# Performance work log

Measured on AMD Instinct MI355X. Metric: run time of the kernel, lower is better.

Reference implementation:

```python
import jax, jax.numpy as jnp
import numpy as np

B, LF, RATE = 2, 2048, 4
DF, DS, H = 1024, 1024, 8
D2 = DF // 2            # 512: both self (d1) and cross (d2) branch dims (equal split)
POOL_H = 2048
TS = LF // RATE         # 512 slow steps


def _p(key, shape):
    return jax.random.normal(key, shape, jnp.float32) * 0.02


def setup_inputs() -> dict:
    keys = iter(jax.random.split(jax.random.key(0), 32))
    inp = {
        "x_fast": jax.random.normal(next(keys), (B, LF, DF), jnp.float32),
        "x_slow": jax.random.normal(next(keys), (B, TS, DS), jnp.float32),
    }
    for name in ("fself", "fcross", "sself", "scross"):
        inp[f"{name}_wqkv"] = _p(next(keys), (D2, 3 * D2))
        inp[f"{name}_bqkv"] = jnp.zeros((3 * D2,), jnp.float32)
        inp[f"{name}_wo"] = _p(next(keys), (D2, D2))
        inp[f"{name}_bo"] = jnp.zeros((D2,), jnp.float32)
    inp["lift_w"] = _p(next(keys), (DS, D2))
    inp["lift_b"] = jnp.zeros((D2,), jnp.float32)
    inp["pool_w1"] = _p(next(keys), (RATE * DF, POOL_H))
    inp["pool_b1"] = jnp.zeros((POOL_H,), jnp.float32)
    inp["pool_w2"] = _p(next(keys), (POOL_H, D2))
    inp["pool_b2"] = jnp.zeros((D2,), jnp.float32)
    return inp


def _mha(q_in, k_in, v_in, wqkv, bqkv, wo, bo):
    """Standard multihead attention with fused in-proj weight [d, 3d]."""
    b, tq, d = q_in.shape
    hd = d // H
    q = q_in @ wqkv[:, :d] + bqkv[:d]
    k = k_in @ wqkv[:, d:2 * d] + bqkv[d:2 * d]
    v = v_in @ wqkv[:, 2 * d:] + bqkv[2 * d:]
    q = q.reshape(b, tq, H, hd)
    k = k.reshape(b, k_in.shape[1], H, hd)
    v = v.reshape(b, v_in.shape[1], H, hd)
    scores = jnp.einsum('bqhd,bkhd->bhqk', q, k) * np.float32(1.0 / np.sqrt(hd))
    w = jax.nn.softmax(scores, axis=-1)
    o = jnp.einsum('bhqk,bkhd->bqhd', w, v).reshape(b, tq, d)
    return o @ wo + bo


def _forward(x_fast, x_slow,
             fself_wqkv, fself_bqkv, fself_wo, fself_bo,
             fcross_wqkv, fcross_bqkv, fcross_wo, fcross_bo,
             sself_wqkv, sself_bqkv, sself_wo, sself_bo,
             scross_wqkv, scross_bqkv, scross_wo, scross_bo,
             lift_w, lift_b, pool_w1, pool_b1, pool_w2, pool_b2):
    b = x_fast.shape[0]
    # ---- fast level: lift slow -> fast timescale (ffn applied before repeat)
    y = jnp.repeat(x_slow @ lift_w + lift_b, RATE, axis=1)          # [B, LF, D2]
    x1, x2 = x_fast[..., :D2], x_fast[..., D2:]
    z_fast = jnp.concatenate([
        _mha(x1, x1, x1, fself_wqkv, fself_bqkv, fself_wo, fself_bo),
        _mha(x2, y, y, fcross_wqkv, fcross_bqkv, fcross_wo, fcross_bo),
    ], axis=-1)
    # ---- slow level: causal block pooling of fast sequence
    blocks = x_fast.reshape(b, TS, RATE * DF)                        # LF == TS*RATE
    s = jax.nn.gelu(blocks @ pool_w1 + pool_b1) @ pool_w2 + pool_b2  # [B, TS, D2]
    # causal shift: prepend zero slow step, drop last (zero in pooled feature dim)
    s = jnp.concatenate([jnp.zeros((b, 1, D2), s.dtype), s[:, :-1]], axis=1)
    s1, s2 = x_slow[..., :D2], x_slow[..., D2:]
    z_slow = jnp.concatenate([
        _mha(s1, s1, s1, sself_wqkv, sself_bqkv, sself_wo, sself_bo),
        _mha(s2, s, s, scross_wqkv, scross_bqkv, scross_wo, scross_bo),
    ], axis=-1)
    return z_fast, z_slow


def reference(x_fast, x_slow,
              fself_wqkv, fself_bqkv, fself_wo, fself_bo,
              fcross_wqkv, fcross_bqkv, fcross_wo, fcross_bo,
              sself_wqkv, sself_bqkv, sself_wo, sself_bo,
              scross_wqkv, scross_bqkv, scross_wo, scross_bo,
              lift_w, lift_b, pool_w1, pool_b1, pool_w2, pool_b2):
    return _forward(x_fast, x_slow,
                    fself_wqkv, fself_bqkv, fself_wo, fself_bo,
                    fcross_wqkv, fcross_bqkv, fcross_wo, fcross_bo,
                    sself_wqkv, sself_bqkv, sself_wo, sself_bo,
                    scross_wqkv, scross_bqkv, scross_wo, scross_bo,
                    lift_w, lift_b, pool_w1, pool_b1, pool_w2, pool_b2)
```

## Files before the change

### kernel.cpp

```cpp
#include <hip/hip_runtime.h>
#include <hip/hip_bf16.h>


typedef __attribute__((ext_vector_type(8))) short bf16x8;
typedef __attribute__((ext_vector_type(4))) float f32x4;
typedef unsigned short u16;
typedef unsigned int u32;

__device__ inline u16 f2bf(float f) {
    __hip_bfloat16 h = __float2bfloat16(f);
    return *reinterpret_cast<u16*>(&h);
}
__device__ inline u32 pack2(float a, float b) {
    return (u32)f2bf(a) | ((u32)f2bf(b) << 16);
}
__device__ inline float bf2f(u16 h) {
    u32 x = ((u32)h) << 16; float f;
    __builtin_memcpy(&f, &x, 4);
    return f;
}
__device__ inline void gld16(const u16* g, u16* l) {
    __builtin_amdgcn_global_load_lds(
        (const __attribute__((address_space(1))) void*)(g),
        (__attribute__((address_space(3))) void*)(l), 16, 0, 0);
}
template <int N>
__device__ inline void wait_vmcnt() {
    if constexpr (N == 0)      asm volatile("s_waitcnt vmcnt(0)" ::: "memory");
    else if constexpr (N == 4) asm volatile("s_waitcnt vmcnt(4)" ::: "memory");
    else if constexpr (N == 8) asm volatile("s_waitcnt vmcnt(8)" ::: "memory");
}

struct GDesc {
    const u16* A; const u16* Bt; const float* bias;
    void* out0; u16* aux0; u16* aux1;
    int lda, ldb, ldc, K, ntx, mode, rshift, tile_end;
};
struct GPack { int n; int pad[3]; GDesc d[8]; };

struct ADesc { const u16* Q; const u16* K; const u16* Vt; u16* O; int Rq, nk, tile_end, q0b; };
struct APack { int n; int pad[3]; ADesc d[2]; };

struct WDesc { const float* src; u16* dst; int ldn, K, tx_, tile_end; };
struct WPack { int n; int pad[3]; WDesc d[12]; };

struct CvtA { const float* a; u16* da; int na8; const float* b; u16* db; };

template <int TMT>
__device__ __forceinline__ void gemm_body(const GPack& pk, int bid, u16* smem)
{
    constexpr int TM = TMT * 16;
    constexpr int W = TMT / 2;
    constexpr int BUF = TM * 64;
    constexpr int NLD = TM / 32 * 2;
    u16* As = smem;
    u16* Bs = smem + 2 * BUF;

    int di = 0;
    while (bid >= pk.d[di].tile_end) ++di;
    const GDesc g = pk.d[di];
    const int base = di ? pk.d[di - 1].tile_end : 0;
    const int local = bid - base;

    const int total = g.tile_end - base;
    const int tpx = total >> 3;
    const int T = (local & 7) * tpx + (local >> 3);
    const int tx = (T >> 2) % g.ntx;
    const int ty = ((T / (g.ntx << 2)) << 2) + (T & 3);
    const int row0 = ty * TM, col0 = tx * TM;

    const int t = threadIdx.x;
    const int wave = t >> 6, lane = t & 63;
    const int l15 = lane & 15, quad = lane >> 4;
    const int wm = (wave >> 1) * W * 16, wn = (wave & 1) * W * 16;

    const int srow = wave * 8 + (lane >> 3);
    const int ssw = (((lane & 7) ^ (lane >> 3))) * 8;
    const u16* Ag = g.A + (long long)(row0 + srow) * g.lda + ssw;
    const u16* Bg = g.Bt + (long long)(col0 + srow) * g.ldb + ssw;

    const int c0 = (quad ^ (l15 & 7)) * 8;

    f32x4 acc[W][W];
#pragma unroll
    for (int i = 0; i < W; ++i)
#pragma unroll
        for (int j = 0; j < W; ++j) {
            acc[i][j][0] = 0.f; acc[i][j][1] = 0.f;
            acc[i][j][2] = 0.f; acc[i][j][3] = 0.f;
        }

    auto stage = [&](int buf, int k0) {
#pragma unroll
        for (int r = 0; r < TM / 32; ++r) {
            gld16(Ag + (long long)r * 32 * g.lda + k0, As + buf * BUF + r * 2048 + wave * 512);
            gld16(Bg + (long long)r * 32 * g.ldb + k0, Bs + buf * BUF + r * 2048 + wave * 512);
        }
    };
    auto compute = [&](int buf) {
        const u16* Ab = As + buf * BUF;
        const u16* Bb = Bs + buf * BUF;
#pragma unroll
        for (int kc = 0; kc < 2; ++kc) {
            const int cc = kc ? (c0 ^ 32) : c0;
            bf16x8 af[W], bfr[W];
#pragma unroll
            for (int i = 0; i < W; ++i) {
                af[i]  = *(const bf16x8*)(Ab + (wm + i * 16 + l15) * 64 + cc);
                bfr[i] = *(const bf16x8*)(Bb + (wn + i * 16 + l15) * 64 + cc);
            }
#pragma unroll
            for (int i = 0; i < W; ++i)
#pragma unroll
                for (int j = 0; j < W; ++j)
                    acc[i][j] = __builtin_amdgcn_mfma_f32_16x16x32_bf16(af[i], bfr[j], acc[i][j], 0, 0, 0);
        }
    };

    const int nt = g.K >> 6;
    stage(0, 0);
    for (int tt = 0; tt < nt; ++tt) {
        const int cur = tt & 1;
        if (tt + 1 < nt) {
            stage(cur ^ 1, (tt + 1) << 6);
            wait_vmcnt<NLD>();
        } else {
            wait_vmcnt<0>();
        }
        __builtin_amdgcn_sched_barrier(0);
        __builtin_amdgcn_s_barrier();
        __builtin_amdgcn_sched_barrier(0);
        compute(cur);
        __builtin_amdgcn_sched_barrier(0);
        __builtin_amdgcn_s_barrier();
    }

    const int rmask = (1 << g.rshift) - 1;
#pragma unroll
    for (int i = 0; i < W; ++i)
#pragma unroll
        for (int j = 0; j < W; ++j)
#pragma unroll
            for (int r = 0; r < 4; ++r) {
                int m = row0 + wm + i * 16 + quad * 4 + r;
                int n = col0 + wn + j * 16 + l15;
                float v = acc[i][j][r];
                if (g.mode != 5) v += g.bias[n];
                if (g.mode == 0) {
                    ((float*)g.out0)[(long long)m * g.ldc + n] = v;
                } else if (g.mode == 1 || g.mode == 5) {
                    ((u16*)g.out0)[(long long)m * g.ldc + n] = f2bf(v);
                } else if (g.mode == 2) {
                    float x3 = v * v * v;
                    v = 0.5f * v * (1.f + tanhf(0.7978845608028654f * (v + 0.044715f * x3)));
                    ((u16*)g.out0)[(long long)m * g.ldc + n] = f2bf(v);
                } else if (g.mode == 3) {
                    u16 h = f2bf(v);
                    if (n < 512) ((u16*)g.out0)[(long long)m * 512 + n] = h;
                    else if (n < 1024) g.aux0[(long long)m * 512 + (n - 512)] = h;
                    else {
                        int d = n - 1024;
                        int bb = m >> g.rshift, rr = m & rmask;
                        g.aux1[((long long)((bb * 8 + (d >> 6)) * 64 + (d & 63)) << g.rshift) + rr] = h;
                    }
                } else if (g.mode == 4) {
                    u16 h = f2bf(v);
                    if (n < 512) ((u16*)g.out0)[(long long)m * 512 + n] = h;
                    else {
                        int d = n - 512;
                        int bb = m >> g.rshift, rr = m & rmask;
                        g.aux1[((long long)((bb * 8 + (d >> 6)) * 64 + (d & 63)) << g.rshift) + rr] = h;
                    }
                } else {
                    int t9 = m & 511;
                    if (t9 != 511) ((u16*)g.out0)[(long long)(m + 1) * g.ldc + n] = f2bf(v);
                    if (t9 == 0)  ((u16*)g.out0)[(long long)m * g.ldc + n] = 0;
                }
            }
}

#define ALD 72

__device__ __forceinline__ void attn_body(const APack& pk, int bid, u16* smem, float prescale)
{
    u16* Qs  = smem;
    u16* Ks  = smem + 4096;
    u16* Vts = smem + 12288;
    u16* Psb = smem + 20480;

    int di = 0;
    while (bid >= pk.d[di].tile_end) ++di;
    const ADesc g = pk.d[di];
    const int base = di ? pk.d[di - 1].tile_end : 0;
    const int local = bid - base;

    const int t = threadIdx.x;
    const int wave = t >> 6, lane = t & 63;
    const int l15 = lane & 15, quad = lane >> 4;
    const int bh = local & 15, b = bh >> 3, h = bh & 7;
    const int q0 = g.q0b + (local >> 4) * 64;
    const int nk = g.nk;

    const int srow = wave * 8 + (lane >> 3);
    const int ssw = (((lane & 7) ^ (lane >> 3))) * 8;
    const int c0 = (quad ^ (l15 & 7)) * 8;

    const u16* Qg = g.Q + ((long long)(b * g.Rq + q0 + srow) << 9) + h * 64 + ssw;
    const u16* Kg = g.K + ((long long)(b * nk + srow) << 9) + h * 64 + ssw;
    const u16* Vg = g.Vt + (long long)bh * 64 * nk + (long long)srow * nk + ssw;

    auto stage = [&](int buf, int kt) {
#pragma unroll
        for (int r = 0; r < 2; ++r) {
            gld16(Kg + ((long long)(kt + r * 32) << 9), Ks + buf * 4096 + r * 2048 + wave * 512);
            gld16(Vg + (long long)r * 32 * nk + kt, Vts + buf * 4096 + r * 2048 + wave * 512);
        }
    };

#pragma unroll
    for (int r = 0; r < 2; ++r)
        gld16(Qg + ((long long)r * 32 << 9), Qs + r * 2048 + wave * 512);
    stage(0, 0);
    wait_vmcnt<4>();
    __builtin_amdgcn_sched_barrier(0);
    __builtin_amdgcn_s_barrier();
    __builtin_amdgcn_sched_barrier(0);

    bf16x8 qf[2];
    qf[0] = *(const bf16x8*)(Qs + (wave * 16 + l15) * 64 + c0);
    qf[1] = *(const bf16x8*)(Qs + (wave * 16 + l15) * 64 + (c0 ^ 32));

    f32x4 Oacc[4];
#pragma unroll
    for (int nt2 = 0; nt2 < 4; ++nt2) { Oacc[nt2][0] = 0.f; Oacc[nt2][1] = 0.f; Oacc[nt2][2] = 0.f; Oacc[nt2][3] = 0.f; }
    float lr[4] = {0.f, 0.f, 0.f, 0.f};

    u16* Pw = Psb + wave * 16 * ALD;

    auto acompute = [&](int buf) {
        const u16* Kb = Ks + buf * 4096;
        const u16* Vb = Vts + buf * 4096;
#pragma unroll
        for (int k16 = 0; k16 < 4; ++k16) {
            f32x4 s;
            s[0] = 0.f; s[1] = 0.f; s[2] = 0.f; s[3] = 0.f;
            bf16x8 kf0 = *(const bf16x8*)(Kb + (k16 * 16 + l15) * 64 + c0);
            bf16x8 kf1 = *(const bf16x8*)(Kb + (k16 * 16 + l15) * 64 + (c0 ^ 32));
            __builtin_amdgcn_s_setprio(1);
            s = __builtin_amdgcn_mfma_f32_16x16x32_bf16(qf[0], kf0, s, 0, 0, 0);
            s = __builtin_amdgcn_mfma_f32_16x16x32_bf16(qf[1], kf1, s, 0, 0, 0);
            __builtin_amdgcn_s_setprio(0);
#pragma unroll
            for (int r = 0; r < 4; ++r) {
                float p = exp2f(s[r] * prescale);
                lr[r] += p;
                Pw[(quad * 4 + r) * ALD + k16 * 16 + l15] = f2bf(p);
            }
        }
        bf16x8 pf0 = *(const bf16x8*)(Pw + l15 * ALD + quad * 8);
        bf16x8 pf1 = *(const bf16x8*)(Pw + l15 * ALD + 32 + quad * 8);
        __builtin_amdgcn_s_setprio(1);
#pragma unroll
        for (int nt2 = 0; nt2 < 4; ++nt2) {
            bf16x8 vf0 = *(const bf16x8*)(Vb + (nt2 * 16 + l15) * 64 + c0);
            bf16x8 vf1 = *(const bf16x8*)(Vb + (nt2 * 16 + l15) * 64 + (c0 ^ 32));
            Oacc[nt2] = __builtin_amdgcn_mfma_f32_16x16x32_bf16(pf0, vf0, Oacc[nt2], 0, 0, 0);
            Oacc[nt2] = __builtin_amdgcn_mfma_f32_16x16x32_bf16(pf1, vf1, Oacc[nt2], 0, 0, 0);
        }
        __builtin_amdgcn_s_setprio(0);
    };

    const int nt = nk >> 6;
    for (int tt = 0; tt < nt; ++tt) {
        const int cur = tt & 1;
        if (tt + 1 < nt) {
            stage(cur ^ 1, (tt + 1) << 6);
            wait_vmcnt<4>();
        } else {
            wait_vmcnt<0>();
        }
        __builtin_amdgcn_sched_barrier(0);
        __builtin_amdgcn_s_barrier();
        __builtin_amdgcn_sched_barrier(0);
        acompute(cur);
        __builtin_amdgcn_sched_barrier(0);
        __builtin_amdgcn_s_barrier();
    }

    float inv[4];
#pragma unroll
    for (int r = 0; r < 4; ++r) {
        float s = lr[r];
#pragma unroll
        for (int off = 1; off < 16; off <<= 1) s += __shfl_xor(s, off);
        inv[r] = 1.f / s;
    }

    u16* Ob = g.O + ((long long)(b * g.Rq + q0 + wave * 16 + quad * 4) << 9) + h * 64;
#pragma unroll
    for (int nt2 = 0; nt2 < 4; ++nt2)
#pragma unroll
        for (int r = 0; r < 4; ++r)
            Ob[(long long)r * 512 + nt2 * 16 + l15] = f2bf(Oacc[nt2][r] * inv[r]);
}

__device__ __forceinline__ void wt_body(const WPack& pk, int bid, u16* smem)
{
    float* T = (float*)smem;
    int di = 0;
    while (bid >= pk.d[di].tile_end) ++di;
    const WDesc g = pk.d[di];
    const int base = di ? pk.d[di - 1].tile_end : 0;
    const int local = bid - base;
    const int k0 = (local % g.tx_) * 64;
    const int n0 = (local / g.tx_) * 64;
    const int t = threadIdx.x;
#pragma unroll
    for (int i = 0; i < 4; ++i) {
        int idx = t + i * 256;
        int r = idx >> 4, c4 = idx & 15;
        float4 v = *(const float4*)(g.src + (long long)(k0 + r) * g.ldn + n0 + c4 * 4);
        T[r * 68 + c4 * 4 + 0] = v.x; T[r * 68 + c4 * 4 + 1] = v.y;
        T[r * 68 + c4 * 4 + 2] = v.z; T[r * 68 + c4 * 4 + 3] = v.w;
    }
    __syncthreads();
#pragma unroll
    for (int i = 0; i < 4; ++i) {
        int idx = t + i * 256;
        int rn = idx >> 4, k4 = idx & 15;
        uint2 u;
        u.x = pack2(T[(k4 * 4 + 0) * 68 + rn], T[(k4 * 4 + 1) * 68 + rn]);
        u.y = pack2(T[(k4 * 4 + 2) * 68 + rn], T[(k4 * 4 + 3) * 68 + rn]);
        *(uint2*)(g.dst + (long long)(n0 + rn) * g.K + k0 + k4 * 4) = u;
    }
}

__device__ __forceinline__ void cvt_body(const CvtA& cv, int bid)
{
    int i = bid * 256 + threadIdx.x;
    const float* s; u16* d;
    if (i < cv.na8) { s = cv.a + (long long)i * 8; d = cv.da + (long long)i * 8; }
    else { s = cv.b + (long long)(i - cv.na8) * 8; d = cv.db + (long long)(i - cv.na8) * 8; }
    float4 x = *(const float4*)s;
    float4 y = *(const float4*)(s + 4);
    uint4 u;
    u.x = pack2(x.x, x.y); u.y = pack2(x.z, x.w);
    u.z = pack2(y.x, y.y); u.w = pack2(y.z, y.w);
    *(uint4*)d = u;
}

template <int TMT>
__global__ __launch_bounds__(256)
void fat_multi(APack ap, GPack gp, WPack wp, CvtA cv,
               int na, int ngm, int nwt, float prescale)
{
    constexpr int GB = 2 * 2 * (TMT * 16 * 64) * 2;
    constexpr int SB = (GB > 50176) ? GB : 50176;
    __shared__ __align__(16) u16 smem[SB / 2];
    int bid = blockIdx.x;
    if (bid < na) { attn_body(ap, bid, smem, prescale); return; }
    bid -= na;
    if (bid < ngm) { gemm_body<TMT>(gp, bid, smem); return; }
    bid -= ngm;
    if (bid < nwt) { wt_body(wp, bid, smem); return; }
    cvt_body(cv, bid - nwt);
}

extern "C" void kernel_launch(void* const* d_in, const int* in_sizes, int n_in,
                              void* d_out, int out_size, void* d_ws, size_t ws_size,
                              hipStream_t stream)
{
    const float* x_fast      = (const float*)d_in[0];
    const float* x_slow      = (const float*)d_in[1];
    const float* fself_wqkv  = (const float*)d_in[2];
    const float* fself_bqkv  = (const float*)d_in[3];
    const float* fself_wo    = (const float*)d_in[4];
    const float* fself_bo    = (const float*)d_in[5];
    const float* fcross_wqkv = (const float*)d_in[6];
    const float* fcross_bqkv = (const float*)d_in[7];
    const float* fcross_wo   = (const float*)d_in[8];
    const float* fcross_bo   = (const float*)d_in[9];
    const float* sself_wqkv  = (const float*)d_in[10];
    const float* sself_bqkv  = (const float*)d_in[11];
    const float* sself_wo    = (const float*)d_in[12];
    const float* sself_bo    = (const float*)d_in[13];
    const float* scross_wqkv = (const float*)d_in[14];
    const float* scross_bqkv = (const float*)d_in[15];
    const float* scross_wo   = (const float*)d_in[16];
    const float* scross_bo   = (const float*)d_in[17];
    const float* lift_w      = (const float*)d_in[18];
    const float* lift_b      = (const float*)d_in[19];
    const float* pool_w1     = (const float*)d_in[20];
    const float* pool_b1     = (const float*)d_in[21];
    const float* pool_w2     = (const float*)d_in[22];
    const float* pool_b2     = (const float*)d_in[23];

    float* out = (float*)d_out;
    float* zf = out;
    float* zs = out + 2LL * 2048 * 1024;

    float* ws = (float*)d_ws;
    u16* pw1T     = (u16*)(ws + 0);
    u16* wqkvT_f  = (u16*)(ws + 4194304);
    u16* wqkvT_c  = (u16*)(ws + 4587520);
    u16* wqkvT_s  = (u16*)(ws + 4980736);
    u16* wqkvT_sc = (u16*)(ws + 5373952);
    u16* liftT    = (u16*)(ws + 5767168);
    u16* pw2T     = (u16*)(ws + 6029312);
    u16* woT_f    = (u16*)(ws + 6553600);
    u16* woT_c    = (u16*)(ws + 6684672);
    u16* woT_s    = (u16*)(ws + 6815744);
    u16* woT_sc   = (u16*)(ws + 6946816);
    u16* xfb      = (u16*)(ws + 7077888);
    u16* xsb      = (u16*)(ws + 9175040);
    u16* q1       = (u16*)(ws + 9699328);
    u16* k1       = (u16*)(ws + 10747904);
    u16* vt1      = (u16*)(ws + 11796480);
    u16* qs       = (u16*)(ws + 12845056);
    u16* ks       = (u16*)(ws + 13107200);
    u16* vts      = (u16*)(ws + 13369344);
    u16* qcs      = (u16*)(ws + 13631488);
    u16* k2    = (u16*)(ws + 0);
    u16* vt2   = (u16*)(ws + 262144);
    u16* sbufS = (u16*)(ws + 524288);
    u16* kcs   = (u16*)(ws + 786432);
    u16* vtcs  = (u16*)(ws + 1048576);
    u16* fo1   = (u16*)(ws + 1310720);
    u16* fo2   = (u16*)(ws + 2359296);
    u16* so1   = (u16*)(ws + 3407872);
    u16* so2   = (u16*)(ws + 3670016);
    u16* q2   = (u16*)(out + 0);
    u16* ybuf = (u16*)(out + 1048576);
    u16* hbuf = (u16*)(out + 1310720);

    const float PRESCALE = 0.125f * 1.4426950408889634f;
    APack a_null{}; GPack g_null{}; WPack w_null{}; CvtA cv_null{};

    auto gl = [&](GPack& p, int i, const u16* A, int lda,
                  const u16* Bt, int ldb, const float* bias,
                  void* out0, int ldc, int M, int N, int K, int mode,
                  u16* aux0, u16* aux1, int rshift, int TM, int& te) {
        te += (M / TM) * (N / TM);
        p.d[i] = GDesc{A, Bt, bias, out0, aux0, aux1,
                       lda, ldb, ldc, K, N / TM, mode, rshift, te};
    };

    {
        WPack wp; wp.n = 11; int te = 0, i = 0;
        auto add = [&](const float* s, u16* d, int ldn, int K, int N) {
            te += (K / 64) * (N / 64);
            wp.d[i++] = WDesc{s, d, ldn, K, K / 64, te};
        };
        add(pool_w1, pw1T, 2048, 4096, 2048);
        add(fself_wqkv, wqkvT_f, 1536, 512, 1536);
        add(fcross_wqkv, wqkvT_c, 1536, 512, 1536);
        add(sself_wqkv, wqkvT_s, 1536, 512, 1536);
        add(scross_wqkv, wqkvT_sc, 1536, 512, 1536);
        add(lift_w, liftT, 512, 1024, 512);
        add(pool_w2, pw2T, 512, 2048, 512);
        add(fself_wo, woT_f, 512, 512, 512);
        add(fcross_wo, woT_c, 512, 512, 512);
        add(sself_wo, woT_s, 512, 512, 512);
        add(scross_wo, woT_sc, 512, 512, 512);
        CvtA cv{x_fast, xfb, 524288, x_slow, xsb};
        hipLaunchKernelGGL(fat_multi<4>, dim3(te + 2560), dim3(256), 0, stream,
                           a_null, g_null, wp, cv, 0, 0, te, PRESCALE);
    }

    {
        GPack p; p.n = 6; int te = 0;
        gl(p, 0, xfb, 4096, pw1T, 4096, pool_b1, hbuf, 2048,
           1024, 2048, 4096, 2, 0, 0, 0, 128, te);
        gl(p, 1, xfb, 1024, wqkvT_f, 512, fself_bqkv, q1, 512,
           4096, 1536, 512, 3, k1, vt1, 11, 128, te);
        gl(p, 2, xfb + 512, 1024, wqkvT_c, 512, fcross_bqkv, q2, 512,
           4096, 512, 512, 1, 0, 0, 0, 128, te);
        gl(p, 3, xsb, 1024, wqkvT_s, 512, sself_bqkv, qs, 512,
           1024, 1536, 512, 3, ks, vts, 9, 128, te);
        gl(p, 4, xsb, 1024, liftT, 1024, lift_b, ybuf, 512,
           1024, 512, 1024, 1, 0, 0, 0, 128, te);
        gl(p, 5, xsb + 512, 1024, wqkvT_sc, 512, scross_bqkv, qcs, 512,
           1024, 512, 512, 1, 0, 0, 0, 128, te);
        hipLaunchKernelGGL(fat_multi<8>, dim3(te), dim3(256), 0, stream,
                           a_null, p, w_null, cv_null, 0, te, 0, PRESCALE);
    }

    {
        APack ap; ap.n = 2;
        ap.d[0] = ADesc{q1, k1, vt1, fo1, 2048, 2048, 256, 0};
        ap.d[1] = ADesc{qs, ks, vts, so1, 512, 512, 384, 0};
        GPack p; p.n = 2; int te = 0;
        gl(p, 0, hbuf, 2048, pw2T, 2048, pool_b2, sbufS, 512,
           1024, 512, 2048, 6, 0, 0, 0, 64, te);
        gl(p, 1, ybuf, 512, wqkvT_c + 512 * 512, 512, fcross_bqkv + 512, k2, 512,
           1024, 1024, 512, 4, 0, vt2, 9, 64, te);
        hipLaunchKernelGGL(fat_multi<4>, dim3(384 + te), dim3(256), 0, stream,
                           ap, p, w_null, cv_null, 384, te, 0, PRESCALE);
    }

    {
        APack ap; ap.n = 2;
        ap.d[0] = ADesc{q1, k1, vt1, fo1, 2048, 2048, 256, 1024};
        ap.d[1] = ADesc{q2, k2, vt2, fo2, 2048, 512, 768, 0};
        GPack p; p.n = 1; int te = 0;
        gl(p, 0, sbufS, 512, wqkvT_sc + 512 * 512, 512, scross_bqkv + 512, kcs, 512,
           1024, 1024, 512, 4, 0, vtcs, 9, 64, te);
        hipLaunchKernelGGL(fat_multi<4>, dim3(768 + te), dim3(256), 0, stream,
                           ap, p, w_null, cv_null, 768, te, 0, PRESCALE);
    }

    {
        APack ap; ap.n = 1;
        ap.d[0] = ADesc{qcs, kcs, vtcs, so2, 512, 512, 128, 0};
        GPack p; p.n = 3; int te = 0;
        gl(p, 0, fo1, 512, woT_f, 512, fself_bo, zf, 1024,
           4096, 512, 512, 0, 0, 0, 0, 64, te);
        gl(p, 1, fo2, 512, woT_c, 512, fcross_bo, zf + 512, 1024,
           4096, 512, 512, 0, 0, 0, 0, 64, te);
        gl(p, 2, so1, 512, woT_s, 512, sself_bo, zs, 1024,
           1024, 512, 512, 0, 0, 0, 0, 64, te);
        hipLaunchKernelGGL(fat_multi<4>, dim3(128 + te), dim3(256), 0, stream,
                           ap, p, w_null, cv_null, 128, te, 0, PRESCALE);
    }

    {
        GPack p; p.n = 1; int te = 0;
        gl(p, 0, so2, 512, woT_sc, 512, scross_bo, zs + 512, 1024,
           1024, 512, 512, 0, 0, 0, 0, 64, te);
        hipLaunchKernelGGL(fat_multi<4>, dim3(te), dim3(256), 0, stream,
                           a_null, p, w_null, cv_null, 0, te, 0, PRESCALE);
    }
}
```

Measured before the change: 332.8 us.

## Reschedule launches so attention starts earlier, overlapping remaining projection GEMMs

Splits the big projection launch so the fast-self and slow-self QKV projections run first on their own. Their attention blocks then run in the next launch alongside the pool, cross-Q and lift GEMMs. The later launches are rebalanced so the second half of fast-self attention runs with the pool2 and k2 GEMMs, and cross attention runs with the kcs GEMM. A flag lets GEMM blocks be dispatched before attention blocks, so longer GEMM tiles start first. This adds one kernel launch and changes per-launch load balance, and it uses TMT=8 GEMM tiles alongside attention in the same launch.

```diff
diff --git a/kernel.cpp b/kernel.cpp
--- a/kernel.cpp
+++ b/kernel.cpp
@@ -352,16 +352,23 @@
 template <int TMT>
 __global__ __launch_bounds__(256)
 void fat_multi(APack ap, GPack gp, WPack wp, CvtA cv,
-               int na, int ngm, int nwt, float prescale)
+               int na, int ngm, int nwt, int attn_first, float prescale)
 {
     constexpr int GB = 2 * 2 * (TMT * 16 * 64) * 2;
     constexpr int SB = (GB > 50176) ? GB : 50176;
     __shared__ __align__(16) u16 smem[SB / 2];
     int bid = blockIdx.x;
-    if (bid < na) { attn_body(ap, bid, smem, prescale); return; }
-    bid -= na;
-    if (bid < ngm) { gemm_body<TMT>(gp, bid, smem); return; }
-    bid -= ngm;
+    if (attn_first) {
+        if (bid < na) { attn_body(ap, bid, smem, prescale); return; }
+        bid -= na;
+        if (bid < ngm) { gemm_body<TMT>(gp, bid, smem); return; }
+        bid -= ngm;
+    } else {
+        if (bid < ngm) { gemm_body<TMT>(gp, bid, smem); return; }
+        bid -= ngm;
+        if (bid < na) { attn_body(ap, bid, smem, prescale); return; }
+        bid -= na;
+    }
     if (bid < nwt) { wt_body(wp, bid, smem); return; }
     cvt_body(cv, bid - nwt);
 }
@@ -464,49 +471,56 @@
         add(scross_wo, woT_sc, 512, 512, 512);
         CvtA cv{x_fast, xfb, 524288, x_slow, xsb};
         hipLaunchKernelGGL(fat_multi<4>, dim3(te + 2560), dim3(256), 0, stream,
-                           a_null, g_null, wp, cv, 0, 0, te, PRESCALE);
-    }
-
-    {
-        GPack p; p.n = 6; int te = 0;
+                           a_null, g_null, wp, cv, 0, 0, te, 0, PRESCALE);
+    }
+
+    {
+        GPack p; p.n = 2; int te = 0;
+        gl(p, 0, xfb, 1024, wqkvT_f, 512, fself_bqkv, q1, 512,
+           4096, 1536, 512, 3, k1, vt1, 11, 128, te);
+        gl(p, 1, xsb, 1024, wqkvT_s, 512, sself_bqkv, qs, 512,
+           1024, 1536, 512, 3, ks, vts, 9, 128, te);
+        hipLaunchKernelGGL(fat_multi<8>, dim3(te), dim3(256), 0, stream,
+                           a_null, p, w_null, cv_null, 0, te, 0, 0, PRESCALE);
+    }
+
+    {
+        GPack p; p.n = 4; int te = 0;
         gl(p, 0, xfb, 4096, pw1T, 4096, pool_b1, hbuf, 2048,
            1024, 2048, 4096, 2, 0, 0, 0, 128, te);
-        gl(p, 1, xfb, 1024, wqkvT_f, 512, fself_bqkv, q1, 512,
-           4096, 1536, 512, 3, k1, vt1, 11, 128, te);
-        gl(p, 2, xfb + 512, 1024, wqkvT_c, 512, fcross_bqkv, q2, 512,
+        gl(p, 1, xfb + 512, 1024, wqkvT_c, 512, fcross_bqkv, q2, 512,
            4096, 512, 512, 1, 0, 0, 0, 128, te);
-        gl(p, 3, xsb, 1024, wqkvT_s, 512, sself_bqkv, qs, 512,
-           1024, 1536, 512, 3, ks, vts, 9, 128, te);
-        gl(p, 4, xsb, 1024, liftT, 1024, lift_b, ybuf, 512,
+        gl(p, 2, xsb, 1024, liftT, 1024, lift_b, ybuf, 512,
            1024, 512, 1024, 1, 0, 0, 0, 128, te);
-        gl(p, 5, xsb + 512, 1024, wqkvT_sc, 512, scross_bqkv, qcs, 512,
+        gl(p, 3, xsb + 512, 1024, wqkvT_sc, 512, scross_bqkv, qcs, 512,
            1024, 512, 512, 1, 0, 0, 0, 128, te);
-        hipLaunchKernelGGL(fat_multi<8>, dim3(te), dim3(256), 0, stream,
-                           a_null, p, w_null, cv_null, 0, te, 0, PRESCALE);
-    }
-
-    {
         APack ap; ap.n = 2;
         ap.d[0] = ADesc{q1, k1, vt1, fo1, 2048, 2048, 256, 0};
         ap.d[1] = ADesc{qs, ks, vts, so1, 512, 512, 384, 0};
+        hipLaunchKernelGGL(fat_multi<8>, dim3(te + 384), dim3(256), 0, stream,
+                           ap, p, w_null, cv_null, 384, te, 0, 0, PRESCALE);
+    }
+
+    {
         GPack p; p.n = 2; int te = 0;
         gl(p, 0, hbuf, 2048, pw2T, 2048, pool_b2, sbufS, 512,
            1024, 512, 2048, 6, 0, 0, 0, 64, te);
         gl(p, 1, ybuf, 512, wqkvT_c + 512 * 512, 512, fcross_bqkv + 512, k2, 512,
            1024, 1024, 512, 4, 0, vt2, 9, 64, te);
-        hipLaunchKernelGGL(fat_multi<4>, dim3(384 + te), dim3(256), 0, stream,
-                           ap, p, w_null, cv_null, 384, te, 0, PRESCALE);
-    }
-
-    {
-        APack ap; ap.n = 2;
+        APack ap; ap.n = 1;
         ap.d[0] = ADesc{q1, k1, vt1, fo1, 2048, 2048, 256, 1024};
-        ap.d[1] = ADesc{q2, k2, vt2, fo2, 2048, 512, 768, 0};
+        hipLaunchKernelGGL(fat_multi<4>, dim3(te + 256), dim3(256), 0, stream,
+                           ap, p, w_null, cv_null, 256, te, 0, 0, PRESCALE);
+    }
+
+    {
         GPack p; p.n = 1; int te = 0;
         gl(p, 0, sbufS, 512, wqkvT_sc + 512 * 512, 512, scross_bqkv + 512, kcs, 512,
            1024, 1024, 512, 4, 0, vtcs, 9, 64, te);
-        hipLaunchKernelGGL(fat_multi<4>, dim3(768 + te), dim3(256), 0, stream,
-                           ap, p, w_null, cv_null, 768, te, 0, PRESCALE);
+        APack ap; ap.n = 1;
+        ap.d[0] = ADesc{q2, k2, vt2, fo2, 2048, 512, 512, 0};
+        hipLaunchKernelGGL(fat_multi<4>, dim3(te + 512), dim3(256), 0, stream,
+                           ap, p, w_null, cv_null, 512, te, 0, 0, PRESCALE);
     }
 
     {
@@ -520,7 +534,7 @@
         gl(p, 2, so1, 512, woT_s, 512, sself_bo, zs, 1024,
            1024, 512, 512, 0, 0, 0, 0, 64, te);
         hipLaunchKernelGGL(fat_multi<4>, dim3(128 + te), dim3(256), 0, stream,
-                           ap, p, w_null, cv_null, 128, te, 0, PRESCALE);
+                           ap, p, w_null, cv_null, 128, te, 0, 1, PRESCALE);
     }
 
     {
@@ -528,6 +542,6 @@
         gl(p, 0, so2, 512, woT_sc, 512, scross_bo, zs + 512, 1024,
            1024, 512, 512, 0, 0, 0, 0, 64, te);
         hipLaunchKernelGGL(fat_multi<4>, dim3(te), dim3(256), 0, stream,
-                           a_null, p, w_null, cv_null, 0, te, 0, PRESCALE);
-    }
-}
+                           a_null, p, w_null, cv_null, 0, te, 0, 0, PRESCALE);
+    }
+}
```

Result: slower. 351.6 us (+5.6%).

## Process 128 query rows per attention block to reuse K/V tiles

Applied to the files above, without the earlier changes.

Each attention block now handles two 64-row query halves, so every staged K/V tile is used twice and the number of attention blocks is halved. Q fragments are loaded straight from global memory into registers instead of going through LDS, which removes the Q shared buffer and the initial barrier. Shared memory per block shrinks, which may allow more blocks per CU. In exchange, register pressure rises and there are fewer blocks to fill the GPU.

```diff
diff --git a/kernel.cpp b/kernel.cpp
--- a/kernel.cpp
+++ b/kernel.cpp
@@ -183,10 +183,9 @@
 
 __device__ __forceinline__ void attn_body(const APack& pk, int bid, u16* smem, float prescale)
 {
-    u16* Qs  = smem;
-    u16* Ks  = smem + 4096;
-    u16* Vts = smem + 12288;
-    u16* Psb = smem + 20480;
+    u16* Ks  = smem;
+    u16* Vts = smem + 8192;
+    u16* Psb = smem + 16384;
 
     int di = 0;
     while (bid >= pk.d[di].tile_end) ++di;
@@ -198,16 +197,25 @@
     const int wave = t >> 6, lane = t & 63;
     const int l15 = lane & 15, quad = lane >> 4;
     const int bh = local & 15, b = bh >> 3, h = bh & 7;
-    const int q0 = g.q0b + (local >> 4) * 64;
+    const int q0 = g.q0b + (local >> 4) * 128;
     const int nk = g.nk;
 
     const int srow = wave * 8 + (lane >> 3);
     const int ssw = (((lane & 7) ^ (lane >> 3))) * 8;
     const int c0 = (quad ^ (l15 & 7)) * 8;
 
-    const u16* Qg = g.Q + ((long long)(b * g.Rq + q0 + srow) << 9) + h * 64 + ssw;
     const u16* Kg = g.K + ((long long)(b * nk + srow) << 9) + h * 64 + ssw;
     const u16* Vg = g.Vt + (long long)bh * 64 * nk + (long long)srow * nk + ssw;
+
+    bf16x8 qf[2][2];
+    {
+        const u16* Qrow = g.Q + ((long long)(b * g.Rq + q0 + wave * 16 + l15) << 9)
+                        + h * 64 + quad * 8;
+        qf[0][0] = *(const bf16x8*)(Qrow);
+        qf[0][1] = *(const bf16x8*)(Qrow + 32);
+        qf[1][0] = *(const bf16x8*)(Qrow + (64LL << 9));
+        qf[1][1] = *(const bf16x8*)(Qrow + (64LL << 9) + 32);
+    }
 
     auto stage = [&](int buf, int kt) {
 #pragma unroll
@@ -217,23 +225,16 @@
         }
     };
 
-#pragma unroll
-    for (int r = 0; r < 2; ++r)
-        gld16(Qg + ((long long)r * 32 << 9), Qs + r * 2048 + wave * 512);
-    stage(0, 0);
-    wait_vmcnt<4>();
-    __builtin_amdgcn_sched_barrier(0);
-    __builtin_amdgcn_s_barrier();
-    __builtin_amdgcn_sched_barrier(0);
-
-    bf16x8 qf[2];
-    qf[0] = *(const bf16x8*)(Qs + (wave * 16 + l15) * 64 + c0);
-    qf[1] = *(const bf16x8*)(Qs + (wave * 16 + l15) * 64 + (c0 ^ 32));
-
-    f32x4 Oacc[4];
-#pragma unroll
-    for (int nt2 = 0; nt2 < 4; ++nt2) { Oacc[nt2][0] = 0.f; Oacc[nt2][1] = 0.f; Oacc[nt2][2] = 0.f; Oacc[nt2][3] = 0.f; }
-    float lr[4] = {0.f, 0.f, 0.f, 0.f};
+    f32x4 Oacc[2][4];
+    float lr[2][4];
+#pragma unroll
+    for (int hf = 0; hf < 2; ++hf)
+#pragma unroll
+        for (int nt2 = 0; nt2 < 4; ++nt2) {
+            Oacc[hf][nt2][0] = 0.f; Oacc[hf][nt2][1] = 0.f;
+            Oacc[hf][nt2][2] = 0.f; Oacc[hf][nt2][3] = 0.f;
+            lr[hf][nt2] = 0.f;
+        }
 
     u16* Pw = Psb + wave * 16 * ALD;
 
@@ -241,35 +242,39 @@
         const u16* Kb = Ks + buf * 4096;
         const u16* Vb = Vts + buf * 4096;
 #pragma unroll
-        for (int k16 = 0; k16 < 4; ++k16) {
-            f32x4 s;
-            s[0] = 0.f; s[1] = 0.f; s[2] = 0.f; s[3] = 0.f;
-            bf16x8 kf0 = *(const bf16x8*)(Kb + (k16 * 16 + l15) * 64 + c0);
-            bf16x8 kf1 = *(const bf16x8*)(Kb + (k16 * 16 + l15) * 64 + (c0 ^ 32));
+        for (int hf = 0; hf < 2; ++hf) {
+#pragma unroll
+            for (int k16 = 0; k16 < 4; ++k16) {
+                f32x4 s;
+                s[0] = 0.f; s[1] = 0.f; s[2] = 0.f; s[3] = 0.f;
+                bf16x8 kf0 = *(const bf16x8*)(Kb + (k16 * 16 + l15) * 64 + c0);
+                bf16x8 kf1 = *(const bf16x8*)(Kb + (k16 * 16 + l15) * 64 + (c0 ^ 32));
+                __builtin_amdgcn_s_setprio(1);
+                s = __builtin_amdgcn_mfma_f32_16x16x32_bf16(qf[hf][0], kf0, s, 0, 0, 0);
+                s = __builtin_amdgcn_mfma_f32_16x16x32_bf16(qf[hf][1], kf1, s, 0, 0, 0);
+                __builtin_amdgcn_s_setprio(0);
+#pragma unroll
+                for (int r = 0; r < 4; ++r) {
+                    float p = exp2f(s[r] * prescale);
+                    lr[hf][r] += p;
+                    Pw[(quad * 4 + r) * ALD + k16 * 16 + l15] = f2bf(p);
+                }
+            }
+            bf16x8 pf0 = *(const bf16x8*)(Pw + l15 * ALD + quad * 8);
+            bf16x8 pf1 = *(const bf16x8*)(Pw + l15 * ALD + 32 + quad * 8);
             __builtin_amdgcn_s_setprio(1);
-            s = __builtin_amdgcn_mfma_f32_16x16x32_bf16(qf[0], kf0, s, 0, 0, 0);
-            s = __builtin_amdgcn_mfma_f32_16x16x32_bf16(qf[1], kf1, s, 0, 0, 0);
+#pragma unroll
+            for (int nt2 = 0; nt2 < 4; ++nt2) {
+                bf16x8 vf0 = *(const bf16x8*)(Vb + (nt2 * 16 + l15) * 64 + c0);
+                bf16x8 vf1 = *(const bf16x8*)(Vb + (nt2 * 16 + l15) * 64 + (c0 ^ 32));
+                Oacc[hf][nt2] = __builtin_amdgcn_mfma_f32_16x16x32_bf16(pf0, vf0, Oacc[hf][nt2], 0, 0, 0);
+                Oacc[hf][nt2] = __builtin_amdgcn_mfma_f32_16x16x32_bf16(pf1, vf1, Oacc[hf][nt2], 0, 0, 0);
+            }
             __builtin_amdgcn_s_setprio(0);
-#pragma unroll
-            for (int r = 0; r < 4; ++r) {
-                float p = exp2f(s[r] * prescale);
-                lr[r] += p;
-                Pw[(quad * 4 + r) * ALD + k16 * 16 + l15] = f2bf(p);
-            }
-        }
-        bf16x8 pf0 = *(const bf16x8*)(Pw + l15 * ALD + quad * 8);
-        bf16x8 pf1 = *(const bf16x8*)(Pw + l15 * ALD + 32 + quad * 8);
-        __builtin_amdgcn_s_setprio(1);
-#pragma unroll
-        for (int nt2 = 0; nt2 < 4; ++nt2) {
-            bf16x8 vf0 = *(const bf16x8*)(Vb + (nt2 * 16 + l15) * 64 + c0);
-            bf16x8 vf1 = *(const bf16x8*)(Vb + (nt2 * 16 + l15) * 64 + (c0 ^ 32));
-            Oacc[nt2] = __builtin_amdgcn_mfma_f32_16x16x32_bf16(pf0, vf0, Oacc[nt2], 0, 0, 0);
-            Oacc[nt2] = __builtin_amdgcn_mfma_f32_16x16x32_bf16(pf1, vf1, Oacc[nt2], 0, 0, 0);
-        }
-        __builtin_amdgcn_s_setprio(0);
+        }
     };
 
+    stage(0, 0);
     const int nt = nk >> 6;
     for (int tt = 0; tt < nt; ++tt) {
         const int cur = tt & 1;
@@ -287,21 +292,23 @@
         __builtin_amdgcn_s_barrier();
     }
 
-    float inv[4];
-#pragma unroll
-    for (int r = 0; r < 4; ++r) {
-        float s = lr[r];
-#pragma unroll
-        for (int off = 1; off < 16; off <<= 1) s += __shfl_xor(s, off);
-        inv[r] = 1.f / s;
-    }
-
-    u16* Ob = g.O + ((long long)(b * g.Rq + q0 + wave * 16 + quad * 4) << 9) + h * 64;
-#pragma unroll
-    for (int nt2 = 0; nt2 < 4; ++nt2)
-#pragma unroll
-        for (int r = 0; r < 4; ++r)
-            Ob[(long long)r * 512 + nt2 * 16 + l15] = f2bf(Oacc[nt2][r] * inv[r]);
+#pragma unroll
+    for (int hf = 0; hf < 2; ++hf) {
+        float inv[4];
+#pragma unroll
+        for (int r = 0; r < 4; ++r) {
+            float s = lr[hf][r];
+#pragma unroll
+            for (int off = 1; off < 16; off <<= 1) s += __shfl_xor(s, off);
+            inv[r] = 1.f / s;
+        }
+        u16* Ob = g.O + ((long long)(b * g.Rq + q0 + hf * 64 + wave * 16 + quad * 4) << 9) + h * 64;
+#pragma unroll
+        for (int nt2 = 0; nt2 < 4; ++nt2)
+#pragma unroll
+            for (int r = 0; r < 4; ++r)
+                Ob[(long long)r * 512 + nt2 * 16 + l15] = f2bf(Oacc[hf][nt2][r] * inv[r]);
+    }
 }
 
 __device__ __forceinline__ void wt_body(const WPack& pk, int bid, u16* smem)
@@ -355,7 +362,7 @@
                int na, int ngm, int nwt, float prescale)
 {
     constexpr int GB = 2 * 2 * (TMT * 16 * 64) * 2;
-    constexpr int SB = (GB > 50176) ? GB : 50176;
+    constexpr int SB = (GB > 41984) ? GB : 41984;
     __shared__ __align__(16) u16 smem[SB / 2];
     int bid = blockIdx.x;
     if (bid < na) { attn_body(ap, bid, smem, prescale); return; }
@@ -487,31 +494,31 @@
 
     {
         APack ap; ap.n = 2;
-        ap.d[0] = ADesc{q1, k1, vt1, fo1, 2048, 2048, 256, 0};
-        ap.d[1] = ADesc{qs, ks, vts, so1, 512, 512, 384, 0};
+        ap.d[0] = ADesc{q1, k1, vt1, fo1, 2048, 2048, 128, 0};
+        ap.d[1] = ADesc{qs, ks, vts, so1, 512, 512, 192, 0};
         GPack p; p.n = 2; int te = 0;
         gl(p, 0, hbuf, 2048, pw2T, 2048, pool_b2, sbufS, 512,
            1024, 512, 2048, 6, 0, 0, 0, 64, te);
         gl(p, 1, ybuf, 512, wqkvT_c + 512 * 512, 512, fcross_bqkv + 512, k2, 512,
            1024, 1024, 512, 4, 0, vt2, 9, 64, te);
-        hipLaunchKernelGGL(fat_multi<4>, dim3(384 + te), dim3(256), 0, stream,
-                           ap, p, w_null, cv_null, 384, te, 0, PRESCALE);
+        hipLaunchKernelGGL(fat_multi<4>, dim3(192 + te), dim3(256), 0, stream,
+                           ap, p, w_null, cv_null, 192, te, 0, PRESCALE);
     }
 
     {
         APack ap; ap.n = 2;
-        ap.d[0] = ADesc{q1, k1, vt1, fo1, 2048, 2048, 256, 1024};
-        ap.d[1] = ADesc{q2, k2, vt2, fo2, 2048, 512, 768, 0};
+        ap.d[0] = ADesc{q1, k1, vt1, fo1, 2048, 2048, 128, 1024};
+        ap.d[1] = ADesc{q2, k2, vt2, fo2, 2048, 512, 384, 0};
         GPack p; p.n = 1; int te = 0;
         gl(p, 0, sbufS, 512, wqkvT_sc + 512 * 512, 512, scross_bqkv + 512, kcs, 512,
            1024, 1024, 512, 4, 0, vtcs, 9, 64, te);
-        hipLaunchKernelGGL(fat_multi<4>, dim3(768 + te), dim3(256), 0, stream,
-                           ap, p, w_null, cv_null, 768, te, 0, PRESCALE);
+        hipLaunchKernelGGL(fat_multi<4>, dim3(384 + te), dim3(256), 0, stream,
+                           ap, p, w_null, cv_null, 384, te, 0, PRESCALE);
     }
 
     {
         APack ap; ap.n = 1;
-        ap.d[0] = ADesc{qcs, kcs, vtcs, so2, 512, 512, 128, 0};
+        ap.d[0] = ADesc{qcs, kcs, vtcs, so2, 512, 512, 64, 0};
         GPack p; p.n = 3; int te = 0;
         gl(p, 0, fo1, 512, woT_f, 512, fself_bo, zf, 1024,
            4096, 512, 512, 0, 0, 0, 0, 64, te);
@@ -519,8 +526,8 @@
            4096, 512, 512, 0, 0, 0, 0, 64, te);
         gl(p, 2, so1, 512, woT_s, 512, sself_bo, zs, 1024,
            1024, 512, 512, 0, 0, 0, 0, 64, te);
-        hipLaunchKernelGGL(fat_multi<4>, dim3(128 + te), dim3(256), 0, stream,
-                           ap, p, w_null, cv_null, 128, te, 0, PRESCALE);
+        hipLaunchKernelGGL(fat_multi<4>, dim3(64 + te), dim3(256), 0, stream,
+                           ap, p, w_null, cv_null, 64, te, 0, PRESCALE);
     }
 
     {
```

Result: slower. 387.8 us (+16.5%).
